# Kernel tuning notes

Hardware: AMD Instinct MI355X
Metric: run time of the kernel (lower is better)

Reference implementation:

```python
import jax, jax.numpy as jnp
import numpy as np
import math

B, H, L = 8, 512, 2048
CH = 1          # channels
D2 = 32         # d_state // 2 (conjugate pairs)
DT_MIN, DT_MAX = 0.001, 0.1


def setup_inputs() -> dict:
    key = jax.random.key(0)
    ks = jax.random.split(key, 7)
    u = jax.random.normal(ks[0], (B, H, L), dtype=jnp.float32)
    # Chebyshev initialization (SimpleS4)
    h_scale = jnp.exp(jnp.arange(H, dtype=jnp.float32) / H * math.log(DT_MAX / DT_MIN))
    angles = jnp.arange(D2, dtype=jnp.float32) * jnp.pi
    theta = jnp.broadcast_to(angles[None, None, :], (CH, H, D2)).astype(jnp.float32) + 0.0
    a = -(jnp.broadcast_to(h_scale[None, :, None], (CH, H, D2)).astype(jnp.float32) + 0.0)
    b = jax.random.normal(ks[1], (CH, H, D2), dtype=jnp.float32)
    c = jax.random.normal(ks[2], (CH, H, D2), dtype=jnp.float32)
    x0 = jax.random.normal(ks[3], (CH, H, D2), dtype=jnp.float32)
    D = jax.random.normal(ks[4], (CH, H), dtype=jnp.float32)
    lim = 1.0 / math.sqrt(CH * H)
    W = jax.random.uniform(ks[5], (H, CH * H), minval=-lim, maxval=lim, dtype=jnp.float32)
    bias = jax.random.uniform(ks[6], (H,), minval=-lim, maxval=lim, dtype=jnp.float32)
    return dict(u=u, a=a, theta=theta, b=b, c=c, x0=x0, D=D, W=W, bias=bias)


def fft_conv(u, f):
    # u: (B,H,L), f: (C,H,L) -> causal conv (B,C,H,L) via zero-padded FFT
    n = 2 * u.shape[-1]
    u_f = jnp.fft.rfft(u, n=n)
    f_f = jnp.fft.rfft(f, n=n)
    y = jnp.fft.irfft(jnp.einsum('bhl,chl->bchl', u_f, f_f), n=n)
    return y[..., : u.shape[-1]]


def s4_forward(u, a, theta, b, c, x0, D, W, bias):
    Bsz, Hd, l = u.shape
    T = 1.0 / (l - 1)                                   # quadrature step
    z = T * jnp.arange(l, dtype=u.dtype)                # (L,)
    aa = -jnp.abs(a)                                    # (C,H,D2) stable decay
    # Vandermonde-like basis: exp(a z) cos(theta z), shape (C,H,D2,L)
    base = jnp.exp(aa[..., None] * z) * jnp.cos(theta[..., None] * z)
    q = b * c                                           # (C,H,D2)
    f = 2.0 * T * jnp.einsum('chd,chdl->chl', q, base)  # SSM kernel (C,H,L)
    y = fft_conv(u, f)                                  # (B,C,H,L)
    # trapezoid-rule endpoint correction
    y = y - 0.5 * (jnp.einsum('ch,bhl->bchl', f[:, :, 0], u)
                   + jnp.einsum('chl,bh->bchl', f, u[:, :, 0]))
    # initial-state contribution (x0 term)
    k0 = 2.0 * jnp.einsum('chd,chdl->chl', c * x0, base)
    y = y + k0[None]
    # skip connection D*u
    y = y + jnp.einsum('ch,bhl->bchl', D, u)
    y = y.reshape(Bsz, CH * Hd, l)                      # (B, C*H, L)
    # NonLinear head: GELU -> pointwise Linear(C*H -> H) (transposed conv1x1)
    y = jax.nn.gelu(y, approximate=False)
    out = jnp.einsum('hf,bfl->bhl', W, y) + bias[None, :, None]
    return out


def reference(u, a, theta, b, c, x0, D, W, bias):
    return s4_forward(u, a, theta, b, c, x0, D, W, bias)
```

## Files before the change

kernel.cpp:

```cpp
#include <hip/hip_runtime.h>
#include <hip/hip_bf16.h>

#define B_  8
#define H_  512
#define L_  2048
#define D2_ 32
#define NC_ 64
#define LC_ 32
#define EP  36

typedef __attribute__((ext_vector_type(8))) short short8;
typedef __attribute__((ext_vector_type(8))) _Float16 half8;
typedef __attribute__((ext_vector_type(2))) _Float16 half2v;
typedef __attribute__((ext_vector_type(4))) float float4v;

__device__ __forceinline__ half2v pk_fma16(half2v a, half2v b, half2v c) {
    return __builtin_elementwise_fma(a, b, c);
}

__device__ __forceinline__ float gelu_fast(float x) {
    float q = x * fmaf(0.044715f, x * x, 1.0f);
    float s = __expf(-1.5957691216057308f * q);
    return __fdividef(x, 1.0f + s);
}

__device__ __forceinline__ unsigned pack_bf16x2(float x, float y) {
    __hip_bfloat162 p = __float22bfloat162_rn(make_float2(x, y));
    return *(unsigned*)&p;
}
__device__ __forceinline__ float2 unpack_bf16x2(unsigned v) {
    __hip_bfloat162 p = *(__hip_bfloat162*)&v;
    return __bfloat1622float2(p);
}
__device__ __forceinline__ unsigned pack_f16x2(float x, float y) {
    auto v = __builtin_amdgcn_cvt_pkrtz(x, y);
    return *(unsigned*)&v;
}

__device__ __forceinline__ void load_lds16(const void* g, void* l) {
    __builtin_amdgcn_global_load_lds((const __attribute__((address_space(1))) unsigned int*)g,
                                     (__attribute__((address_space(3))) unsigned int*)l, 16, 0, 0);
}

__global__ void cast_prep_kernel(const float* __restrict__ W, __hip_bfloat16* __restrict__ Wb,
                                 const float* __restrict__ a, const float* __restrict__ th,
                                 const float* __restrict__ bb, const float* __restrict__ cc,
                                 const float* __restrict__ x0,
                                 float* __restrict__ aT, float* __restrict__ thT,
                                 float* __restrict__ qT, float* __restrict__ gxT,
                                 _Float16* __restrict__ WPh) {
    int tid = blockIdx.x * 256 + threadIdx.x;
    Wb[tid] = __float2bfloat16(W[tid]);
    if (tid < H_ * D2_) {
        int h = tid & (H_ - 1);
        int d = tid >> 9;
        const float T = 1.0f / (float)(L_ - 1);
        float av = -fabsf(a[h * D2_ + d]);
        float tv = th[h * D2_ + d];
        float q  = bb[h * D2_ + d] * cc[h * D2_ + d];
        aT[tid]  = av;
        thT[tid] = tv;
        qT[tid]  = q;
        gxT[tid] = 2.0f * cc[h * D2_ + d] * x0[h * D2_ + d];
        #pragma unroll
        for (int k = 0; k < 6; ++k) {
            float len = (float)(32 << k);
            float e2  = __expf(av * T * len);
            float an  = tv * T * len;
            WPh[((size_t)h * 6 + k) * 64 + d]      = (_Float16)(e2 * __cosf(an));
            WPh[((size_t)h * 6 + k) * 64 + 32 + d] = (_Float16)(e2 * __sinf(an));
        }
    }
}

__global__ __launch_bounds__(256) void fkprep_kernel(
        const float* __restrict__ aT, const float* __restrict__ thT,
        const float* __restrict__ qT, const float* __restrict__ gxT,
        unsigned* __restrict__ FKf, _Float16* __restrict__ AB,
        _Float16* __restrict__ CB) {
    __shared__ float f_lds[32];
    int h = blockIdx.x;
    int t = threadIdx.x;
    int q4 = t & 3, lc = t >> 2;
    const float T = 1.0f / (float)(L_ - 1);
    float z0 = T * (float)(lc * 32);
    float pr[8], pi[8], wr[8], wi[8], qd[8], gx[8];
    #pragma unroll
    for (int j = 0; j < 8; ++j) {
        int idx = (q4 * 8 + j) * H_ + h;
        float aa = aT[idx], tv = thT[idx];
        float e0 = __expf(aa * z0);
        pr[j] = e0 * __cosf(tv * z0);
        pi[j] = e0 * __sinf(tv * z0);
        float e1 = __expf(aa * T);
        wr[j] = e1 * __cosf(tv * T);
        wi[j] = e1 * __sinf(tv * T);
        qd[j] = qT[idx];
        gx[j] = gxT[idx];
    }
    for (int i = 0; i < 32; ++i) {
        float fa = 0.f, ka = 0.f;
        #pragma unroll
        for (int j = 0; j < 8; ++j) {
            fa = fmaf(qd[j], pr[j], fa);
            ka = fmaf(gx[j], pr[j], ka);
            float nr = fmaf(pr[j], wr[j], -(pi[j] * wi[j]));
            float ni = fmaf(pr[j], wi[j],  (pi[j] * wr[j]));
            pr[j] = nr; pi[j] = ni;
        }
        fa += __shfl_xor(fa, 1); fa += __shfl_xor(fa, 2);
        ka += __shfl_xor(ka, 1); ka += __shfl_xor(ka, 2);
        if (q4 == 0) {
            float fv = 2.0f * T * fa;
            FKf[(size_t)h * L_ + lc * 32 + i] = pack_bf16x2(fv, ka);
            if (lc == 0) f_lds[i] = fv;
        }
    }
    __syncthreads();
    for (int e = t; e < 64 * 32; e += 256) {
        int m = e >> 5, i = e & 31;
        int d = m & 31;
        float av = aT[d * H_ + h], tv = thT[d * H_ + h];
        float z  = T * (float)(31 - i);
        float ex = __expf(av * z);
        float v  = (m < 32) ? ex * __cosf(tv * z) : ex * __sinf(tv * z);
        AB[(size_t)h * 2048 + e] = (_Float16)v;
    }
    for (int e = t; e < 32 * 96; e += 256) {
        int i = e / 96, k = e - i * 96;
        float v = 0.f;
        if (k < 32) {
            if (k <= i) v = f_lds[i - k];
        } else {
            int d = (k < 64) ? k - 32 : k - 64;
            float av = aT[d * H_ + h], tv = thT[d * H_ + h];
            float qs = 2.0f * T * qT[d * H_ + h];
            float z  = T * (float)(i + 1);
            float ex = __expf(av * z);
            v = (k < 64) ? qs * ex * __cosf(tv * z) : -qs * ex * __sinf(tv * z);
        }
        CB[(size_t)h * 3072 + e] = (_Float16)v;
    }
}

__global__ __launch_bounds__(128, 6) void scan_mfma_kernel(
        const float* __restrict__ u, const _Float16* __restrict__ AB,
        const _Float16* __restrict__ CB, const unsigned* __restrict__ WPh,
        const float* __restrict__ Dp, const unsigned* __restrict__ FKf,
        __hip_bfloat16* __restrict__ y) {
    __shared__ __align__(16) unsigned El[64 * EP];
    int wid = threadIdx.x >> 6, lane = threadIdx.x & 63;
    int h = blockIdx.x, b = blockIdx.y;
    int ln = lane & 15, qq = lane >> 4;
    const float* ug = u + (size_t)(b * H_ + h) * L_;

    half8 uf[4];
    #pragma unroll
    for (int nb = 0; nb < 4; ++nb) {
        const float* p = ug + (nb * 16 + ln) * 32 + qq * 8;
        float4 a0 = *(const float4*)p;
        float4 a1 = *(const float4*)(p + 4);
        unsigned* vp = (unsigned*)&uf[nb];
        vp[0] = pack_f16x2(a0.x, a0.y);
        vp[1] = pack_f16x2(a0.z, a0.w);
        vp[2] = pack_f16x2(a1.x, a1.y);
        vp[3] = pack_f16x2(a1.z, a1.w);
    }

    const _Float16* ABh = AB + (size_t)h * 2048;
    int j0 = wid * 8 + qq * 2;
    #pragma unroll
    for (int e = 0; e < 2; ++e) {
        half8 af = *(const half8*)&ABh[(e * 32 + wid * 16 + ln) * 32 + qq * 8];
        #pragma unroll
        for (int nb = 0; nb < 4; ++nb) {
            float4v acc = (float4v){0.f, 0.f, 0.f, 0.f};
            acc = __builtin_amdgcn_mfma_f32_16x16x32_f16(af, uf[nb], acc, 0, 0, 0);
            unsigned p0 = pack_f16x2(acc[0], acc[1]);
            unsigned p1 = pack_f16x2(acc[2], acc[3]);
            *(uint2*)&El[(nb * 16 + ln) * EP + e * 16 + j0] = make_uint2(p0, p1);
        }
    }
    asm volatile("s_waitcnt lgkmcnt(0)" ::: "memory");
    __builtin_amdgcn_sched_barrier(0);

    int c = lane;
    unsigned sr[8], si[8];
    {
        const unsigned* rp = &El[c * EP + wid * 8];
        uint4 r0 = *(const uint4*)rp;
        uint4 r1 = *(const uint4*)(rp + 4);
        uint4 i0 = *(const uint4*)(rp + 16);
        uint4 i1 = *(const uint4*)(rp + 20);
        sr[0]=r0.x; sr[1]=r0.y; sr[2]=r0.z; sr[3]=r0.w;
        sr[4]=r1.x; sr[5]=r1.y; sr[6]=r1.z; sr[7]=r1.w;
        si[0]=i0.x; si[1]=i0.y; si[2]=i0.z; si[3]=i0.w;
        si[4]=i1.x; si[5]=i1.y; si[6]=i1.z; si[7]=i1.w;
    }
    const unsigned* mpb = WPh + (size_t)h * 6 * 32;
    #pragma unroll
    for (int st = 0; st < 6; ++st) {
        int off = 1 << st;
        int src = (c - off) & 63;
        bool act = c >= off;
        const unsigned* mp = mpb + st * 32 + wid * 8;
        #pragma unroll
        for (int jj = 0; jj < 8; ++jj) {
            unsigned prp = (unsigned)__shfl((int)sr[jj], src);
            unsigned pip = (unsigned)__shfl((int)si[jj], src);
            if (!act) { prp = 0u; pip = 0u; }
            unsigned mru = mp[jj];
            unsigned miu = mp[16 + jj];
            unsigned min_ = miu ^ 0x80008000u;
            half2v pr = *(half2v*)&prp, pi = *(half2v*)&pip;
            half2v Mr = *(half2v*)&mru, Mi = *(half2v*)&miu, Mni = *(half2v*)&min_;
            half2v s_r = *(half2v*)&sr[jj], s_i = *(half2v*)&si[jj];
            half2v nr = pk_fma16(pr, Mr, pk_fma16(pi, Mni, s_r));
            half2v ni = pk_fma16(pr, Mi, pk_fma16(pi, Mr,  s_i));
            sr[jj] = *(unsigned*)&nr; si[jj] = *(unsigned*)&ni;
        }
    }
    {
        int srcm1 = (c - 1) & 63;
        #pragma unroll
        for (int jj = 0; jj < 8; ++jj) {
            unsigned a0 = (unsigned)__shfl((int)sr[jj], srcm1);
            unsigned b0 = (unsigned)__shfl((int)si[jj], srcm1);
            if (c == 0) { a0 = 0u; b0 = 0u; }
            sr[jj] = a0; si[jj] = b0;
        }
    }
    {
        unsigned* wp = &El[c * EP + wid * 8];
        *(uint4*)wp        = make_uint4(sr[0], sr[1], sr[2], sr[3]);
        *(uint4*)(wp + 4)  = make_uint4(sr[4], sr[5], sr[6], sr[7]);
        *(uint4*)(wp + 16) = make_uint4(si[0], si[1], si[2], si[3]);
        *(uint4*)(wp + 20) = make_uint4(si[4], si[5], si[6], si[7]);
    }
    const unsigned* fgh = FKf + (size_t)h * L_;
    uint4 fkp[2][2];
    #pragma unroll
    for (int nbi = 0; nbi < 2; ++nbi) {
        int col = (2 * wid + nbi) * 16 + ln;
        fkp[nbi][0] = *(const uint4*)&fgh[col * 32 + qq * 4];
        fkp[nbi][1] = *(const uint4*)&fgh[col * 32 + 16 + qq * 4];
    }
    __syncthreads();

    const _Float16* CBh = CB + (size_t)h * 3072;
    float4v acc2[2][2];
    #pragma unroll
    for (int mb = 0; mb < 2; ++mb)
        #pragma unroll
        for (int nbi = 0; nbi < 2; ++nbi)
            acc2[mb][nbi] = (float4v){0.f, 0.f, 0.f, 0.f};
    #pragma unroll
    for (int ks = 0; ks < 3; ++ks) {
        half8 a2[2];
        a2[0] = *(const half8*)&CBh[(ln)      * 96 + ks * 32 + qq * 8];
        a2[1] = *(const half8*)&CBh[(16 + ln) * 96 + ks * 32 + qq * 8];
        #pragma unroll
        for (int nbi = 0; nbi < 2; ++nbi) {
            int col = (2 * wid + nbi) * 16 + ln;
            half8 bfv;
            if (ks == 0) bfv = uf[2 * wid + nbi];
            else {
                int off = (ks == 1) ? 0 : 16;
                bfv = *(const half8*)&El[col * EP + off + qq * 4];
            }
            acc2[0][nbi] = __builtin_amdgcn_mfma_f32_16x16x32_f16(a2[0], bfv, acc2[0][nbi], 0, 0, 0);
            acc2[1][nbi] = __builtin_amdgcn_mfma_f32_16x16x32_f16(a2[1], bfv, acc2[1][nbi], 0, 0, 0);
        }
    }

    float f0; { f0 = unpack_bf16x2(fgh[0]).x; }
    float c0v = Dp[h] - 0.5f * f0;
    float c1v = -0.5f * ug[0];
    #pragma unroll
    for (int nbi = 0; nbi < 2; ++nbi) {
        int col = (2 * wid + nbi) * 16 + ln;
        #pragma unroll
        for (int mb = 0; mb < 2; ++mb) {
            int l0 = col * 32 + mb * 16 + qq * 4;
            float4 u4 = *(const float4*)(ug + l0);
            uint4 fkv = fkp[nbi][mb];
            float us[4] = {u4.x, u4.y, u4.z, u4.w};
            unsigned fs[4] = {fkv.x, fkv.y, fkv.z, fkv.w};
            float g[4];
            #pragma unroll
            for (int r = 0; r < 4; ++r) {
                float2 fk = unpack_bf16x2(fs[r]);
                float yv = acc2[mb][nbi][r] + fmaf(c0v, us[r], fmaf(c1v, fk.x, fk.y));
                g[r] = gelu_fast(yv);
            }
            uint2 yo;
            yo.x = pack_bf16x2(g[0], g[1]);
            yo.y = pack_bf16x2(g[2], g[3]);
            *(uint2*)((short*)y + (size_t)(b * H_ + h) * L_ + l0) = yo;
        }
    }
}

__global__ __launch_bounds__(256) void transpose_y_kernel(
        const __hip_bfloat16* __restrict__ y, __hip_bfloat16* __restrict__ yT) {
    __shared__ short tile[64][72];
    int l0 = blockIdx.x * 64, f0 = blockIdx.y * 64, b = blockIdx.z;
    int t = threadIdx.x;
    int row = t >> 3, col8 = (t & 7) * 8;
    const short* yg = (const short*)y + (size_t)b * H_ * L_;
    #pragma unroll
    for (int r2 = 0; r2 < 64; r2 += 32)
        *(uint4*)&tile[row + r2][col8] =
            *(const uint4*)&yg[(size_t)(f0 + row + r2) * L_ + l0 + col8];
    __syncthreads();
    short* og = (short*)yT + (size_t)b * L_ * H_;
    #pragma unroll
    for (int r2 = 0; r2 < 64; r2 += 32) {
        int lrow = row + r2;
        short v[8];
        #pragma unroll
        for (int j = 0; j < 8; ++j) v[j] = tile[col8 + j][lrow];
        *(uint4*)&og[(size_t)(l0 + lrow) * H_ + f0 + col8] = *(uint4*)v;
    }
}

__global__ __launch_bounds__(256) void gemm_kernel(
        const __hip_bfloat16* __restrict__ Wb, const __hip_bfloat16* __restrict__ yT,
        const float* __restrict__ bias, float* __restrict__ out) {
    __shared__ __align__(16) short As[64 * 32];
    __shared__ __align__(16) short Bs[128 * 32];
    int l0 = blockIdx.x * 128;
    int h0 = blockIdx.y * 64;
    int b  = blockIdx.z;
    int t    = threadIdx.x;
    int lane = t & 63, wave = t >> 6;
    int m_off = (wave >> 1) * 32, n_off = (wave & 1) * 64;
    int quad = lane >> 4, ln = lane & 15;

    float4v acc[2][4];
    #pragma unroll
    for (int mt = 0; mt < 2; ++mt)
        #pragma unroll
        for (int nt = 0; nt < 4; ++nt)
            acc[mt][nt] = (float4v){0.f, 0.f, 0.f, 0.f};

    const short* Wg = (const short*)Wb;
    const short* Yg = (const short*)(yT + (size_t)b * L_ * H_);

    int r  = t >> 2;
    int qd = t & 3;

    for (int kt = 0; kt < 16; ++kt) {
        int k0 = kt * 32;
        load_lds16(Wg + (h0 + r) * 512 + k0 + qd * 8, &As[t * 8]);
        load_lds16(Yg + (size_t)(l0 + r)      * 512 + k0 + qd * 8, &Bs[t * 8]);
        load_lds16(Yg + (size_t)(l0 + r + 64) * 512 + k0 + qd * 8, &Bs[(t + 256) * 8]);
        __syncthreads();

        short8 af[2], bf[4];
        #pragma unroll
        for (int mt = 0; mt < 2; ++mt)
            af[mt] = *(const short8*)&As[(m_off + mt * 16 + ln) * 32 + quad * 8];
        #pragma unroll
        for (int nt = 0; nt < 4; ++nt)
            bf[nt] = *(const short8*)&Bs[(n_off + nt * 16 + ln) * 32 + quad * 8];
        #pragma unroll
        for (int mt = 0; mt < 2; ++mt)
            #pragma unroll
            for (int nt = 0; nt < 4; ++nt)
                acc[mt][nt] = __builtin_amdgcn_mfma_f32_16x16x32_bf16(
                    af[mt], bf[nt], acc[mt][nt], 0, 0, 0);
        __syncthreads();
    }

    #pragma unroll
    for (int mt = 0; mt < 2; ++mt) {
        #pragma unroll
        for (int nt = 0; nt < 4; ++nt) {
            int hh = h0 + m_off + mt * 16 + quad * 4;
            int ll = l0 + n_off + nt * 16 + ln;
            #pragma unroll
            for (int r2 = 0; r2 < 4; ++r2)
                out[((size_t)(b * H_ + hh + r2)) * L_ + ll] = acc[mt][nt][r2] + bias[hh + r2];
        }
    }
}

extern "C" void kernel_launch(void* const* d_in, const int* in_sizes, int n_in,
                              void* d_out, int out_size, void* d_ws, size_t ws_size,
                              hipStream_t stream) {
    const float* u    = (const float*)d_in[0];
    const float* a    = (const float*)d_in[1];
    const float* th   = (const float*)d_in[2];
    const float* bb   = (const float*)d_in[3];
    const float* cc   = (const float*)d_in[4];
    const float* x0   = (const float*)d_in[5];
    const float* Dp   = (const float*)d_in[6];
    const float* W    = (const float*)d_in[7];
    const float* bias = (const float*)d_in[8];
    float* out = (float*)d_out;
    char* ws = (char*)d_ws;

    unsigned*       FKf = (unsigned*)ws;
    __hip_bfloat16* yT  = (__hip_bfloat16*)(ws + (4ull  << 20));
    __hip_bfloat16* y   = (__hip_bfloat16*)(ws + (20ull << 20));
    __hip_bfloat16* Wb  = (__hip_bfloat16*)(ws + (36ull << 20));
    _Float16*       AB  = (_Float16*)(ws + (37ull << 20));
    _Float16*       CB  = (_Float16*)(ws + (39ull << 20));
    float* pbase = (float*)(ws + (42ull << 20));
    float *aT  = pbase,           *thT = pbase + 16384, *qT = pbase + 2*16384,
          *gxT = pbase + 3*16384;
    _Float16* WPh = (_Float16*)(pbase + 4*16384);

    hipLaunchKernelGGL(cast_prep_kernel,  dim3(1024),      dim3(256), 0, stream,
                       W, Wb, a, th, bb, cc, x0, aT, thT, qT, gxT, WPh);
    hipLaunchKernelGGL(fkprep_kernel,     dim3(H_),        dim3(256), 0, stream,
                       aT, thT, qT, gxT, FKf, AB, CB);
    hipLaunchKernelGGL(scan_mfma_kernel,  dim3(H_, B_),    dim3(128), 0, stream,
                       u, AB, CB, (const unsigned*)WPh, Dp, FKf, y);
    hipLaunchKernelGGL(transpose_y_kernel,dim3(32, 8, 8),  dim3(256), 0, stream, y, yT);
    hipLaunchKernelGGL(gemm_kernel,       dim3(16, 8, 8),  dim3(256), 0, stream,
                       Wb, yT, bias, out);
}
```

Baseline: 171.9 us.

## Fuse cast/prep into fkprep, raise scan occupancy, swizzle transpose LDS tile

Result: no change. 169.4 us (-1.5%).

```diff
diff --git a/kernel.cpp b/kernel.cpp
--- a/kernel.cpp
+++ b/kernel.cpp
@@ -42,26 +42,26 @@
                                      (__attribute__((address_space(3))) unsigned int*)l, 16, 0, 0);
 }
 
-__global__ void cast_prep_kernel(const float* __restrict__ W, __hip_bfloat16* __restrict__ Wb,
-                                 const float* __restrict__ a, const float* __restrict__ th,
-                                 const float* __restrict__ bb, const float* __restrict__ cc,
-                                 const float* __restrict__ x0,
-                                 float* __restrict__ aT, float* __restrict__ thT,
-                                 float* __restrict__ qT, float* __restrict__ gxT,
-                                 _Float16* __restrict__ WPh) {
-    int tid = blockIdx.x * 256 + threadIdx.x;
-    Wb[tid] = __float2bfloat16(W[tid]);
-    if (tid < H_ * D2_) {
-        int h = tid & (H_ - 1);
-        int d = tid >> 9;
-        const float T = 1.0f / (float)(L_ - 1);
+__global__ __launch_bounds__(256) void fkprep_kernel(
+        const float* __restrict__ a, const float* __restrict__ th,
+        const float* __restrict__ bb, const float* __restrict__ cc,
+        const float* __restrict__ x0, const float* __restrict__ W,
+        __hip_bfloat16* __restrict__ Wb, unsigned* __restrict__ FKf,
+        _Float16* __restrict__ AB, _Float16* __restrict__ CB,
+        _Float16* __restrict__ WPh) {
+    __shared__ float avs[32], tvs[32], qds[32], gxs[32], f_lds[32];
+    int h = blockIdx.x;
+    int t = threadIdx.x;
+    const float T = 1.0f / (float)(L_ - 1);
+    Wb[(size_t)h * 512 + t]       = __float2bfloat16(W[(size_t)h * 512 + t]);
+    Wb[(size_t)h * 512 + t + 256] = __float2bfloat16(W[(size_t)h * 512 + t + 256]);
+    if (t < 32) {
+        int d = t;
         float av = -fabsf(a[h * D2_ + d]);
         float tv = th[h * D2_ + d];
-        float q  = bb[h * D2_ + d] * cc[h * D2_ + d];
-        aT[tid]  = av;
-        thT[tid] = tv;
-        qT[tid]  = q;
-        gxT[tid] = 2.0f * cc[h * D2_ + d] * x0[h * D2_ + d];
+        avs[d] = av; tvs[d] = tv;
+        qds[d] = bb[h * D2_ + d] * cc[h * D2_ + d];
+        gxs[d] = 2.0f * cc[h * D2_ + d] * x0[h * D2_ + d];
         #pragma unroll
         for (int k = 0; k < 6; ++k) {
             float len = (float)(32 << k);
@@ -71,32 +71,22 @@
             WPh[((size_t)h * 6 + k) * 64 + 32 + d] = (_Float16)(e2 * __sinf(an));
         }
     }
-}
-
-__global__ __launch_bounds__(256) void fkprep_kernel(
-        const float* __restrict__ aT, const float* __restrict__ thT,
-        const float* __restrict__ qT, const float* __restrict__ gxT,
-        unsigned* __restrict__ FKf, _Float16* __restrict__ AB,
-        _Float16* __restrict__ CB) {
-    __shared__ float f_lds[32];
-    int h = blockIdx.x;
-    int t = threadIdx.x;
+    __syncthreads();
     int q4 = t & 3, lc = t >> 2;
-    const float T = 1.0f / (float)(L_ - 1);
     float z0 = T * (float)(lc * 32);
     float pr[8], pi[8], wr[8], wi[8], qd[8], gx[8];
     #pragma unroll
     for (int j = 0; j < 8; ++j) {
-        int idx = (q4 * 8 + j) * H_ + h;
-        float aa = aT[idx], tv = thT[idx];
+        int d = q4 * 8 + j;
+        float aa = avs[d], tv = tvs[d];
         float e0 = __expf(aa * z0);
         pr[j] = e0 * __cosf(tv * z0);
         pi[j] = e0 * __sinf(tv * z0);
         float e1 = __expf(aa * T);
         wr[j] = e1 * __cosf(tv * T);
         wi[j] = e1 * __sinf(tv * T);
-        qd[j] = qT[idx];
-        gx[j] = gxT[idx];
+        qd[j] = qds[d];
+        gx[j] = gxs[d];
     }
     for (int i = 0; i < 32; ++i) {
         float fa = 0.f, ka = 0.f;
@@ -120,7 +110,7 @@
     for (int e = t; e < 64 * 32; e += 256) {
         int m = e >> 5, i = e & 31;
         int d = m & 31;
-        float av = aT[d * H_ + h], tv = thT[d * H_ + h];
+        float av = avs[d], tv = tvs[d];
         float z  = T * (float)(31 - i);
         float ex = __expf(av * z);
         float v  = (m < 32) ? ex * __cosf(tv * z) : ex * __sinf(tv * z);
@@ -133,8 +123,8 @@
             if (k <= i) v = f_lds[i - k];
         } else {
             int d = (k < 64) ? k - 32 : k - 64;
-            float av = aT[d * H_ + h], tv = thT[d * H_ + h];
-            float qs = 2.0f * T * qT[d * H_ + h];
+            float av = avs[d], tv = tvs[d];
+            float qs = 2.0f * T * qds[d];
             float z  = T * (float)(i + 1);
             float ex = __expf(av * z);
             v = (k < 64) ? qs * ex * __cosf(tv * z) : -qs * ex * __sinf(tv * z);
@@ -143,7 +133,7 @@
     }
 }
 
-__global__ __launch_bounds__(128, 6) void scan_mfma_kernel(
+__global__ __launch_bounds__(128, 8) void scan_mfma_kernel(
         const float* __restrict__ u, const _Float16* __restrict__ AB,
         const _Float16* __restrict__ CB, const unsigned* __restrict__ WPh,
         const float* __restrict__ Dp, const unsigned* __restrict__ FKf,
@@ -309,9 +299,11 @@
     int row = t >> 3, col8 = (t & 7) * 8;
     const short* yg = (const short*)y + (size_t)b * H_ * L_;
     #pragma unroll
-    for (int r2 = 0; r2 < 64; r2 += 32)
-        *(uint4*)&tile[row + r2][col8] =
-            *(const uint4*)&yg[(size_t)(f0 + row + r2) * L_ + l0 + col8];
+    for (int r2 = 0; r2 < 64; r2 += 32) {
+        int fr = row + r2;
+        *(uint4*)&tile[fr][col8 ^ (8 * ((fr >> 3) & 7))] =
+            *(const uint4*)&yg[(size_t)(f0 + fr) * L_ + l0 + col8];
+    }
     __syncthreads();
     short* og = (short*)yT + (size_t)b * L_ * H_;
     #pragma unroll
@@ -319,7 +311,10 @@
         int lrow = row + r2;
         short v[8];
         #pragma unroll
-        for (int j = 0; j < 8; ++j) v[j] = tile[col8 + j][lrow];
+        for (int j = 0; j < 8; ++j) {
+            int f = col8 + j;
+            v[j] = tile[f][lrow ^ (8 * ((f >> 3) & 7))];
+        }
         *(uint4*)&og[(size_t)(l0 + lrow) * H_ + f0 + col8] = *(uint4*)v;
     }
 }
@@ -407,15 +402,10 @@
     __hip_bfloat16* Wb  = (__hip_bfloat16*)(ws + (36ull << 20));
     _Float16*       AB  = (_Float16*)(ws + (37ull << 20));
     _Float16*       CB  = (_Float16*)(ws + (39ull << 20));
-    float* pbase = (float*)(ws + (42ull << 20));
-    float *aT  = pbase,           *thT = pbase + 16384, *qT = pbase + 2*16384,
-          *gxT = pbase + 3*16384;
-    _Float16* WPh = (_Float16*)(pbase + 4*16384);
-
-    hipLaunchKernelGGL(cast_prep_kernel,  dim3(1024),      dim3(256), 0, stream,
-                       W, Wb, a, th, bb, cc, x0, aT, thT, qT, gxT, WPh);
+    _Float16*       WPh = (_Float16*)(ws + (42ull << 20));
+
     hipLaunchKernelGGL(fkprep_kernel,     dim3(H_),        dim3(256), 0, stream,
-                       aT, thT, qT, gxT, FKf, AB, CB);
+                       a, th, bb, cc, x0, W, Wb, FKf, AB, CB, WPh);
     hipLaunchKernelGGL(scan_mfma_kernel,  dim3(H_, B_),    dim3(128), 0, stream,
                        u, AB, CB, (const unsigned*)WPh, Dp, FKf, y);
     hipLaunchKernelGGL(transpose_y_kernel,dim3(32, 8, 8),  dim3(256), 0, stream, y, yT);
```
